# Kernel optimization log

Hardware: AMD Instinct MI355X
Metric: run time of the kernel (lower is better)

## Reference

```python
import jax, jax.numpy as jnp
import numpy as np
from jax import lax

T, B, H, NF, FS = 512, 128, 512, 128, 5  # max_seq_len, batch, hidden, num_filters, filter_size


def setup_inputs() -> dict:
    key = jax.random.key(0)
    ks = jax.random.split(key, 16)
    inp = {
        "encoder_output": jax.random.normal(ks[0], (T, B, H), dtype=jnp.float32),
        "lengths": jax.random.randint(ks[1], (B,), 1, T + 1, dtype=jnp.int64 if jax.config.jax_enable_x64 else jnp.int32),
    }
    for w in range(1, FS + 1):
        inp[f"conv_w{w}"] = jax.random.normal(ks[1 + w], (NF, 1, H, w), dtype=jnp.float32) * 0.02
        inp[f"conv_b{w}"] = jnp.zeros((NF,), dtype=jnp.float32)
    inp["fc1_w"] = jax.random.normal(ks[12], (100, FS * NF), dtype=jnp.float32) * 0.05
    inp["fc1_b"] = jnp.zeros((100,), dtype=jnp.float32)
    inp["fc2_w"] = jax.random.normal(ks[13], (1, 100), dtype=jnp.float32) * 0.1
    inp["fc2_b"] = jnp.zeros((1,), dtype=jnp.float32)
    return inp


def _raw_reshape(x, L):
    # Faithful to torch .contiguous().view(1,1,H,-1) on a [L,H] slice:
    # row-major flatten of first L rows, reshaped to [H, L], zero-padded to [H, T].
    flat = x.reshape(-1)                       # [T*H]
    h = jnp.arange(H)[:, None]                 # [H,1]
    l = jnp.arange(T)[None, :]                 # [1,T]
    return jnp.where(l < L, flat[h * L + l], 0.0)  # [H,T]


def reference(encoder_output, lengths,
              conv_w1, conv_b1, conv_w2, conv_b2, conv_w3, conv_b3,
              conv_w4, conv_b4, conv_w5, conv_b5,
              fc1_w, fc1_b, fc2_w, fc2_b):
    # encoder_output: [T, B, H]; per-sample raw reshape to [H, T] (length-dependent)
    X = jax.vmap(_raw_reshape, in_axes=(1, 0))(encoder_output, lengths)  # [B,H,T]
    X4 = X[:, None, :, :]                                               # [B,1,H,T]
    Leff = jnp.maximum(lengths, FS)  # torch code zero-pads width to >= filter_size
    conv_ws = [conv_w1, conv_w2, conv_w3, conv_w4, conv_w5]
    conv_bs = [conv_b1, conv_b2, conv_b3, conv_b4, conv_b5]
    pools = []
    for w in range(1, FS + 1):
        out = lax.conv_general_dilated(
            X4, conv_ws[w - 1], window_strides=(1, 1), padding='VALID',
            dimension_numbers=('NCHW', 'OIHW', 'NCHW'))          # [B,NF,1,T-w+1]
        r = jax.nn.relu(out[:, :, 0, :] + conv_bs[w - 1][None, :, None])  # [B,NF,Tw]
        tpos = jnp.arange(T - w + 1)
        valid = tpos[None, :] < (Leff - w + 1)[:, None]          # [B,Tw]
        r = jnp.where(valid[:, None, :], r, 0.0)                 # relu>=0, so 0 is safe for max
        pools.append(r.max(axis=2))                              # [B,NF]
    feat = jnp.concatenate(pools, axis=1)                        # [B,FS*NF]
    fc1 = feat @ fc1_w.T + fc1_b
    fc2 = fc1 @ fc2_w.T + fc2_b
    probs = jax.nn.sigmoid(fc2)                                  # [B,1]
    return probs[:, None, :]                                     # [B,1,1] == torch.stack of [1,1]
```

## Files before the change

### kernel.cpp

```cpp
#include <hip/hip_runtime.h>
#include <hip/hip_bf16.h>

#define TT 512
#define BB 128
#define HH 512
#define NFC 128

typedef short v8s __attribute__((ext_vector_type(8)));
typedef float v4f __attribute__((ext_vector_type(4)));

__device__ __forceinline__ unsigned short f2bf(float x) {
    unsigned u = __float_as_uint(x);
    unsigned r = (u + 0x7fffu + ((u >> 16) & 1u)) >> 16;
    return (unsigned short)r;
}

__global__ void prep_all(const float* __restrict__ enc, const int* __restrict__ lengths,
                         unsigned short* __restrict__ Xg,
                         const float* __restrict__ w1, const float* __restrict__ w2,
                         const float* __restrict__ w3, const float* __restrict__ w4,
                         const float* __restrict__ w5, unsigned short* __restrict__ Wg,
                         float* __restrict__ pools,
                         const float* __restrict__ fc1w, const float* __restrict__ fc1b,
                         const float* __restrict__ fc2w, const float* __restrict__ fc2b,
                         float* __restrict__ v, int* __restrict__ wl) {
    int blk = blockIdx.x;
    int tid = threadIdx.x;
    if (blk < 8192) {
        __shared__ float tile[64 * 65];
        int b = blk >> 6;
        int lc = (blk >> 3) & 7;
        int hc = blk & 7;
        int L = lengths[b];
        int Leff = L > 5 ? L : 5;
        int l0 = lc * 64, h0 = hc * 64;
        if (l0 >= Leff + 127) return;
        int lx = tid & 63;
        int hq = tid >> 6;
        #pragma unroll
        for (int r = 0; r < 16; ++r) {
            int hl = hq * 16 + r;
            int l = l0 + lx;
            float val = 0.f;
            if (l < L) {
                int i = (h0 + hl) * L + l;
                val = enc[(i >> 9) * (BB * HH) + b * HH + (i & 511)];
            }
            tile[hl * 65 + lx] = val;
        }
        __syncthreads();
        int hg = tid & 15;
        #pragma unroll
        for (int r = 0; r < 4; ++r) {
            int lloc = (tid >> 4) + r * 16;
            int n = b * 512 + l0 + lloc;
            ushort4 pk;
            pk.x = f2bf(tile[(hg * 4 + 0) * 65 + lloc]);
            pk.y = f2bf(tile[(hg * 4 + 1) * 65 + lloc]);
            pk.z = f2bf(tile[(hg * 4 + 2) * 65 + lloc]);
            pk.w = f2bf(tile[(hg * 4 + 3) * 65 + lloc]);
            *(ushort4*)&Xg[n * 512 + h0 + hg * 4] = pk;
        }
    } else if (blk < 12288) {
        int idx = (blk - 8192) * 256 + tid;
        int s = idx >> 9, h = idx & 511;
        int f = s >> 4, sl = s & 15;
        float val = 0.f;
        if (sl < 15) {
            int w, j;
            if (sl < 1)       { w = 1; j = sl; }
            else if (sl < 3)  { w = 2; j = sl - 1; }
            else if (sl < 6)  { w = 3; j = sl - 3; }
            else if (sl < 10) { w = 4; j = sl - 6; }
            else              { w = 5; j = sl - 10; }
            const float* wp = (w == 1) ? w1 : (w == 2) ? w2 : (w == 3) ? w3 : (w == 4) ? w4 : w5;
            val = wp[f * (HH * w) + h * w + j];
        }
        Wg[idx] = f2bf(val);
    } else if (blk < 12608) {
        int i = (blk - 12288) * 256 + tid;
        if (i < BB * 5 * NFC) pools[i] = 0.f;
    } else if (blk == 12608) {
        for (int k = tid; k < 640; k += 256) {
            float s = 0.f;
            for (int o = 0; o < 100; ++o) s += fc2w[o] * fc1w[o * 640 + k];
            v[k] = s;
        }
        if (tid == 0) {
            float c = fc2b[0];
            for (int o = 0; o < 100; ++o) c += fc2w[o] * fc1b[o];
            v[640] = c;
        }
    } else {
        if (tid == 0) {
            int cnt = 0;
            for (int b = 0; b < BB; ++b) {
                int L = lengths[b];
                int Leff = L > 5 ? L : 5;
                for (int tt = 0; tt < 5; ++tt) {
                    int n0 = tt * 124 - ((tt >> 2) * 112);
                    if (n0 < Leff) wl[cnt++] = (b << 3) | tt;
                }
            }
            wl[640] = cnt;
        }
    }
}

__global__ __launch_bounds__(256, 2)
void conv_gemm(const unsigned short* __restrict__ Wg, const unsigned short* __restrict__ Xg,
               const int* __restrict__ lengths, const int* __restrict__ wl,
               const float* __restrict__ cb1, const float* __restrict__ cb2,
               const float* __restrict__ cb3, const float* __restrict__ cb4,
               const float* __restrict__ cb5,
               float* __restrict__ pools) {
    __shared__ __align__(16) char smem[24576];
    unsigned short* ldsA = (unsigned short*)smem;
    unsigned short* ldsB = (unsigned short*)(smem + 16384);
    float* Gs = (float*)smem;

    int cnt = wl[640];
    int wk = blockIdx.x;
    if (wk >= cnt) return;
    int item = wl[wk];
    int b = item >> 3, tt = item & 7;
    int mt = blockIdx.y;
    int n0 = tt * 124 - ((tt >> 2) * 112);
    int L = lengths[b];
    int Leff = L > 5 ? L : 5;

    int tid = threadIdx.x;
    int wid = tid >> 6, lane = tid & 63;
    int wm = wid >> 1, wn = wid & 1;
    int llo = lane & 15, quad = lane >> 4;
    int psw = quad ^ ((llo >> 1) & 3);

    int m0 = mt * 256;
    int nb0 = b * 512 + n0;

    v4f acc[8][4];
    #pragma unroll
    for (int i = 0; i < 8; ++i)
        #pragma unroll
        for (int j = 0; j < 4; ++j) acc[i][j] = v4f{0.f, 0.f, 0.f, 0.f};

    int srow = lane >> 2;
    int gchunk = (lane & 3) ^ ((lane >> 3) & 3);
    const unsigned short* gA = Wg + (m0 + wid * 64 + srow) * 512 + gchunk * 8;
    const unsigned short* gB = Xg + (nb0 + wid * 32 + srow) * 512 + gchunk * 8;

    #pragma unroll 1
    for (int kt = 0; kt < 16; ++kt) {
        int ko = kt * 32;
        #pragma unroll
        for (int q = 0; q < 4; ++q)
            __builtin_amdgcn_global_load_lds(
                (const __attribute__((address_space(1))) unsigned int*)(gA + q * (16 * 512) + ko),
                (__attribute__((address_space(3))) unsigned int*)&ldsA[(wid * 64 + q * 16) * 32],
                16, 0, 0);
        #pragma unroll
        for (int q = 0; q < 2; ++q)
            __builtin_amdgcn_global_load_lds(
                (const __attribute__((address_space(1))) unsigned int*)(gB + q * (16 * 512) + ko),
                (__attribute__((address_space(3))) unsigned int*)&ldsB[(wid * 32 + q * 16) * 32],
                16, 0, 0);
        __syncthreads();
        v8s Af[8], Bf[4];
        #pragma unroll
        for (int mi = 0; mi < 8; ++mi)
            Af[mi] = *(const v8s*)&ldsA[(wm * 128 + mi * 16 + llo) * 32 + psw * 8];
        #pragma unroll
        for (int ni = 0; ni < 4; ++ni)
            Bf[ni] = *(const v8s*)&ldsB[(wn * 64 + ni * 16 + llo) * 32 + psw * 8];
        #pragma unroll
        for (int mi = 0; mi < 8; ++mi)
            #pragma unroll
            for (int ni = 0; ni < 4; ++ni)
                acc[mi][ni] = __builtin_amdgcn_mfma_f32_16x16x32_bf16(Af[mi], Bf[ni], acc[mi][ni], 0, 0, 0);
        __syncthreads();
    }

    const int basew[6] = {0, 0, 1, 3, 6, 10};
    int fg = wid & 1, half = wid >> 1;
    int tcol = half * 64 + lane;

    #pragma unroll
    for (int p = 0; p < 8; ++p) {
        if (wm == (p >> 2)) {
            #pragma unroll
            for (int mi2 = 0; mi2 < 2; ++mi2)
                #pragma unroll
                for (int ni = 0; ni < 4; ++ni)
                    #pragma unroll
                    for (int r = 0; r < 4; ++r)
                        Gs[(mi2 * 16 + quad * 4 + r) * 129 + wn * 64 + ni * 16 + llo] =
                            acc[(p & 3) * 2 + mi2][ni][r];
        }
        __syncthreads();
        {
            int f = mt * 16 + p * 2 + fg;
            #pragma unroll
            for (int w = 1; w <= 5; ++w) {
                float bias = (w == 1 ? cb1 : w == 2 ? cb2 : w == 3 ? cb3 : w == 4 ? cb4 : cb5)[f];
                int limv = Leff - w + 1 - n0;
                float vmax = -1.f;
                if (tcol <= 128 - w && tcol < limv) {
                    float s = 0.f;
                    #pragma unroll
                    for (int j = 0; j < w; ++j)
                        s += Gs[(fg * 16 + basew[w] + j) * 129 + tcol + j];
                    s += bias;
                    vmax = fmaxf(s, 0.f);
                }
                #pragma unroll
                for (int off = 32; off >= 1; off >>= 1)
                    vmax = fmaxf(vmax, __shfl_xor(vmax, off));
                if (lane == 0 && vmax >= 0.f)
                    atomicMax((int*)&pools[(b * 5 + (w - 1)) * NFC + f], __float_as_int(vmax));
            }
        }
        __syncthreads();
    }
}

__global__ void head(const float* __restrict__ pools, const float* __restrict__ v,
                     float* __restrict__ out) {
    int b = blockIdx.x;
    int tid = threadIdx.x;
    float s = 0.f;
    for (int k = tid; k < 640; k += 256) s += pools[b * 640 + k] * v[k];
    __shared__ float red[256];
    red[tid] = s;
    __syncthreads();
    for (int st = 128; st; st >>= 1) {
        if (tid < st) red[tid] += red[tid + st];
        __syncthreads();
    }
    if (tid == 0) out[b] = 1.f / (1.f + expf(-(red[0] + v[640])));
}

extern "C" void kernel_launch(void* const* d_in, const int* in_sizes, int n_in,
                              void* d_out, int out_size, void* d_ws, size_t ws_size,
                              hipStream_t stream) {
    const float* enc  = (const float*)d_in[0];
    const int* lens   = (const int*)d_in[1];
    const float* w1   = (const float*)d_in[2];
    const float* b1   = (const float*)d_in[3];
    const float* w2   = (const float*)d_in[4];
    const float* b2   = (const float*)d_in[5];
    const float* w3   = (const float*)d_in[6];
    const float* b3   = (const float*)d_in[7];
    const float* w4   = (const float*)d_in[8];
    const float* b4   = (const float*)d_in[9];
    const float* w5   = (const float*)d_in[10];
    const float* b5   = (const float*)d_in[11];
    const float* fc1w = (const float*)d_in[12];
    const float* fc1b = (const float*)d_in[13];
    const float* fc2w = (const float*)d_in[14];
    const float* fc2b = (const float*)d_in[15];
    float* out = (float*)d_out;

    unsigned short* Xg = (unsigned short*)d_ws;
    unsigned short* Wg = Xg + 33554432;
    float* pools  = (float*)(Wg + 1048576);
    float* vbuf   = pools + 81920;
    int* wlist    = (int*)(vbuf + 641);

    prep_all<<<12610, 256, 0, stream>>>(enc, lens, Xg, w1, w2, w3, w4, w5, Wg, pools,
                                        fc1w, fc1b, fc2w, fc2b, vbuf, wlist);
    conv_gemm<<<dim3(640, 8), 256, 0, stream>>>(Wg, Xg, lens, wlist, b1, b2, b3, b4, b5, pools);
    head<<<128, 256, 0, stream>>>(pools, vbuf, out);
}
```

Measured before the change: 423.0 us.

## Halve conv GEMM M-tile, load B fragments directly from global, parallelize worklist

The conv GEMM M-tile shrinks from 256 to 128 rows, the grid doubles in y, and launch bounds rise to 4 blocks per CU to raise occupancy. B fragments are now read straight from global memory into registers instead of being staged through LDS, and the epilogue processes one filter per wave in two phases. The worklist build in prep_all is spread across threads with a shared atomic counter rather than run by a single thread. This trades more redundant global reads of X (each X tile is now read by twice as many blocks) and non-coalesced fragment loads for lower register and LDS pressure. Worklist order also becomes nondeterministic.

```diff
diff --git a/kernel.cpp b/kernel.cpp
--- a/kernel.cpp
+++ b/kernel.cpp
@@ -92,31 +92,33 @@
             v[640] = c;
         }
     } else {
-        if (tid == 0) {
-            int cnt = 0;
-            for (int b = 0; b < BB; ++b) {
-                int L = lengths[b];
-                int Leff = L > 5 ? L : 5;
-                for (int tt = 0; tt < 5; ++tt) {
-                    int n0 = tt * 124 - ((tt >> 2) * 112);
-                    if (n0 < Leff) wl[cnt++] = (b << 3) | tt;
-                }
+        __shared__ int cnt;
+        if (tid == 0) cnt = 0;
+        __syncthreads();
+        for (int it = tid; it < 640; it += 256) {
+            int b = it / 5, tt = it % 5;
+            int L = lengths[b];
+            int Leff = L > 5 ? L : 5;
+            int n0 = tt * 124 - ((tt >> 2) * 112);
+            if (n0 < Leff) {
+                int pos = atomicAdd(&cnt, 1);
+                wl[pos] = (b << 3) | tt;
             }
-            wl[640] = cnt;
-        }
-    }
-}
-
-__global__ __launch_bounds__(256, 2)
+        }
+        __syncthreads();
+        if (tid == 0) wl[640] = cnt;
+    }
+}
+
+__global__ __launch_bounds__(256, 4)
 void conv_gemm(const unsigned short* __restrict__ Wg, const unsigned short* __restrict__ Xg,
                const int* __restrict__ lengths, const int* __restrict__ wl,
                const float* __restrict__ cb1, const float* __restrict__ cb2,
                const float* __restrict__ cb3, const float* __restrict__ cb4,
                const float* __restrict__ cb5,
                float* __restrict__ pools) {
-    __shared__ __align__(16) char smem[24576];
+    __shared__ __align__(16) char smem[64 * 129 * 4];
     unsigned short* ldsA = (unsigned short*)smem;
-    unsigned short* ldsB = (unsigned short*)(smem + 16384);
     float* Gs = (float*)smem;
 
     int cnt = wl[640];
@@ -135,45 +137,44 @@
     int llo = lane & 15, quad = lane >> 4;
     int psw = quad ^ ((llo >> 1) & 3);
 
-    int m0 = mt * 256;
+    int m0 = mt * 128;
     int nb0 = b * 512 + n0;
 
-    v4f acc[8][4];
+    v4f acc[4][4];
     #pragma unroll
-    for (int i = 0; i < 8; ++i)
+    for (int i = 0; i < 4; ++i)
         #pragma unroll
         for (int j = 0; j < 4; ++j) acc[i][j] = v4f{0.f, 0.f, 0.f, 0.f};
 
     int srow = lane >> 2;
     int gchunk = (lane & 3) ^ ((lane >> 3) & 3);
-    const unsigned short* gA = Wg + (m0 + wid * 64 + srow) * 512 + gchunk * 8;
-    const unsigned short* gB = Xg + (nb0 + wid * 32 + srow) * 512 + gchunk * 8;
+    const unsigned short* gA = Wg + (m0 + wid * 32 + srow) * 512 + gchunk * 8;
+
+    const unsigned short* pB[4];
+    #pragma unroll
+    for (int ni = 0; ni < 4; ++ni)
+        pB[ni] = Xg + (nb0 + wn * 64 + ni * 16 + llo) * 512 + quad * 8;
 
     #pragma unroll 1
     for (int kt = 0; kt < 16; ++kt) {
         int ko = kt * 32;
-        #pragma unroll
-        for (int q = 0; q < 4; ++q)
+        v8s Bf[4];
+        #pragma unroll
+        for (int ni = 0; ni < 4; ++ni)
+            Bf[ni] = *(const v8s*)(pB[ni] + ko);
+        #pragma unroll
+        for (int q = 0; q < 2; ++q)
             __builtin_amdgcn_global_load_lds(
                 (const __attribute__((address_space(1))) unsigned int*)(gA + q * (16 * 512) + ko),
-                (__attribute__((address_space(3))) unsigned int*)&ldsA[(wid * 64 + q * 16) * 32],
+                (__attribute__((address_space(3))) unsigned int*)&ldsA[(wid * 32 + q * 16) * 32],
                 16, 0, 0);
-        #pragma unroll
-        for (int q = 0; q < 2; ++q)
-            __builtin_amdgcn_global_load_lds(
-                (const __attribute__((address_space(1))) unsigned int*)(gB + q * (16 * 512) + ko),
-                (__attribute__((address_space(3))) unsigned int*)&ldsB[(wid * 32 + q * 16) * 32],
-                16, 0, 0);
-        __syncthreads();
-        v8s Af[8], Bf[4];
-        #pragma unroll
-        for (int mi = 0; mi < 8; ++mi)
-            Af[mi] = *(const v8s*)&ldsA[(wm * 128 + mi * 16 + llo) * 32 + psw * 8];
-        #pragma unroll
-        for (int ni = 0; ni < 4; ++ni)
-            Bf[ni] = *(const v8s*)&ldsB[(wn * 64 + ni * 16 + llo) * 32 + psw * 8];
-        #pragma unroll
-        for (int mi = 0; mi < 8; ++mi)
+        __syncthreads();
+        v8s Af[4];
+        #pragma unroll
+        for (int mi = 0; mi < 4; ++mi)
+            Af[mi] = *(const v8s*)&ldsA[(wm * 64 + mi * 16 + llo) * 32 + psw * 8];
+        #pragma unroll
+        for (int mi = 0; mi < 4; ++mi)
             #pragma unroll
             for (int ni = 0; ni < 4; ++ni)
                 acc[mi][ni] = __builtin_amdgcn_mfma_f32_16x16x32_bf16(Af[mi], Bf[ni], acc[mi][ni], 0, 0, 0);
@@ -181,36 +182,39 @@
     }
 
     const int basew[6] = {0, 0, 1, 3, 6, 10};
-    int fg = wid & 1, half = wid >> 1;
-    int tcol = half * 64 + lane;
 
     #pragma unroll
-    for (int p = 0; p < 8; ++p) {
-        if (wm == (p >> 2)) {
+    for (int phase = 0; phase < 2; ++phase) {
+        if (wm == phase) {
             #pragma unroll
-            for (int mi2 = 0; mi2 < 2; ++mi2)
+            for (int mi = 0; mi < 4; ++mi)
                 #pragma unroll
                 for (int ni = 0; ni < 4; ++ni)
                     #pragma unroll
                     for (int r = 0; r < 4; ++r)
-                        Gs[(mi2 * 16 + quad * 4 + r) * 129 + wn * 64 + ni * 16 + llo] =
-                            acc[(p & 3) * 2 + mi2][ni][r];
+                        Gs[(mi * 16 + quad * 4 + r) * 129 + wn * 64 + ni * 16 + llo] = acc[mi][ni][r];
         }
         __syncthreads();
         {
-            int f = mt * 16 + p * 2 + fg;
+            int fl = wid;
+            int f = mt * 8 + phase * 4 + fl;
             #pragma unroll
             for (int w = 1; w <= 5; ++w) {
                 float bias = (w == 1 ? cb1 : w == 2 ? cb2 : w == 3 ? cb3 : w == 4 ? cb4 : cb5)[f];
                 int limv = Leff - w + 1 - n0;
                 float vmax = -1.f;
-                if (tcol <= 128 - w && tcol < limv) {
-                    float s = 0.f;
-                    #pragma unroll
-                    for (int j = 0; j < w; ++j)
-                        s += Gs[(fg * 16 + basew[w] + j) * 129 + tcol + j];
-                    s += bias;
-                    vmax = fmaxf(s, 0.f);
+                #pragma unroll
+                for (int half = 0; half < 2; ++half) {
+                    int t = half * 64 + lane;
+                    if (t <= 128 - w && t < limv) {
+                        float s = 0.f;
+                        #pragma unroll
+                        for (int j = 0; j < w; ++j)
+                            s += Gs[(fl * 16 + basew[w] + j) * 129 + t + j];
+                        s += bias;
+                        s = fmaxf(s, 0.f);
+                        vmax = fmaxf(vmax, s);
+                    }
                 }
                 #pragma unroll
                 for (int off = 32; off >= 1; off >>= 1)
@@ -268,6 +272,6 @@
 
     prep_all<<<12610, 256, 0, stream>>>(enc, lens, Xg, w1, w2, w3, w4, w5, Wg, pools,
                                         fc1w, fc1b, fc2w, fc2b, vbuf, wlist);
-    conv_gemm<<<dim3(640, 8), 256, 0, stream>>>(Wg, Xg, lens, wlist, b1, b2, b3, b4, b5, pools);
+    conv_gemm<<<dim3(640, 16), 256, 0, stream>>>(Wg, Xg, lens, wlist, b1, b2, b3, b4, b5, pools);
     head<<<128, 256, 0, stream>>>(pools, vbuf, out);
 }
```

Result: slower. 447.6 us (+5.8%).
